# Performance work log

Hardware: AMD Instinct MI355X
Metric: run time of the kernel (lower is better)

Reference implementation:

```python
import jax, jax.numpy as jnp
import numpy as np

DIM = 512
HEADS = 8
DIM_HEAD = 64
INNER = HEADS * DIM_HEAD  # 512
NUM_PATCHES = 64
NUM_FRAMES = 32
EPS = 1e-5


def setup_inputs() -> dict:
    key = jax.random.key(0)
    k1, k2, k3, k4 = jax.random.split(key, 4)
    B, T = 4, NUM_PATCHES * NUM_FRAMES  # 4, 2048
    x = jax.random.normal(k1, (B, T, DIM), dtype=jnp.float32)
    w_qkv = jax.random.normal(k2, (DIM, 3 * INNER), dtype=jnp.float32) * (DIM ** -0.5)
    w_out = jax.random.normal(k3, (INNER, DIM), dtype=jnp.float32) * (INNER ** -0.5)
    b_out = jax.random.normal(k4, (DIM,), dtype=jnp.float32) * 0.01
    ln_g = jnp.ones((DIM,), dtype=jnp.float32)
    ln_b = jnp.zeros((DIM,), dtype=jnp.float32)
    return {"x": x, "ln_g": ln_g, "ln_b": ln_b, "w_qkv": w_qkv, "w_out": w_out, "b_out": b_out}


def _frame_causal_mask(T):
    # token i belongs to frame i // NUM_PATCHES; query frame attends to frames <= its own
    frame = jnp.arange(T) // NUM_PATCHES
    return frame[:, None] >= frame[None, :]  # [T, T] bool


def reference(x, ln_g, ln_b, w_qkv, w_out, b_out):
    B, T, C = x.shape
    scale = DIM_HEAD ** -0.5
    # LayerNorm
    mu = jnp.mean(x, axis=-1, keepdims=True)
    var = jnp.mean(jnp.square(x - mu), axis=-1, keepdims=True)
    xn = (x - mu) * jax.lax.rsqrt(var + EPS) * ln_g + ln_b
    # QKV projection (no bias)
    qkv = xn @ w_qkv  # [B, T, 3*INNER]
    q, k, v = jnp.split(qkv, 3, axis=-1)
    reshape = lambda t: t.reshape(B, T, HEADS, DIM_HEAD).transpose(0, 2, 1, 3)  # b h n d
    q, k, v = reshape(q), reshape(k), reshape(v)
    dots = jnp.einsum('bhqd,bhkd->bhqk', q, k) * scale
    mask = _frame_causal_mask(T)
    dots = jnp.where(mask[None, None], dots, -jnp.inf)
    attn = jax.nn.softmax(dots, axis=-1)
    out = jnp.einsum('bhqk,bhkd->bhqd', attn, v)
    out = out.transpose(0, 2, 1, 3).reshape(B, T, INNER)
    return out @ w_out + b_out
```

## Files before the change

kernel.cpp:

```cpp
#include <hip/hip_runtime.h>

typedef unsigned short u16;
typedef float f32x4 __attribute__((ext_vector_type(4)));
typedef short bf16x8 __attribute__((ext_vector_type(8)));

#define MFMA16(a, b, c) __builtin_amdgcn_mfma_f32_16x16x32_bf16((a), (b), (c), 0, 0, 0)
#define SWZ8(row, off) ((off) ^ (((row) & 7) << 3))

#define CFENCE() asm volatile("" ::: "memory")
#define BARRIER() do { CFENCE(); __builtin_amdgcn_s_barrier(); CFENCE(); } while (0)
#define VMW(n) asm volatile("s_waitcnt vmcnt(" #n ")" ::: "memory")

static __device__ __forceinline__ u16 f2bf(float f) {
  union { float f; unsigned u; } c; c.f = f;
  unsigned r = c.u + 0x7fffu + ((c.u >> 16) & 1u);
  return (u16)(r >> 16);
}

static __device__ __forceinline__ float exp2_hw(float x) {
  float r;
  asm("v_exp_f32 %0, %1" : "=v"(r) : "v"(x));
  return r;
}

static __device__ __forceinline__ unsigned cvtpk(float lo, float hi) {
  unsigned r;
  asm("v_cvt_pk_bf16_f32 %0, %1, %2" : "=v"(r) : "v"(lo), "v"(hi));
  return r;
}

static __device__ __forceinline__ void llds16(u16* l, const u16* g) {
  __builtin_amdgcn_global_load_lds((const __attribute__((address_space(1))) void*)g,
                                   (__attribute__((address_space(3))) void*)l, 16, 0, 0);
}

__global__ __launch_bounds__(256) void prep_weights(
    const float* __restrict__ w_qkv, const float* __restrict__ w_out,
    u16* __restrict__ wqkvT, u16* __restrict__ woutT) {
  __shared__ u16 tile[64][66];
  int bid = blockIdx.x;
  const float* src;
  u16* dst;
  int C, tr, tc;
  if (bid < 192) {
    src = w_qkv; dst = wqkvT; C = 1536;
    tr = (bid & 7) * 64;
    tc = (bid >> 3) * 64;
  } else {
    int b2 = bid - 192;
    src = w_out; dst = woutT; C = 512;
    tr = (b2 & 7) * 64;
    tc = (b2 >> 3) * 64;
  }
  int tid = threadIdx.x;
  int i = tid >> 4;
  int j4 = (tid & 15) * 4;
#pragma unroll
  for (int p = 0; p < 4; ++p) {
    int row = i + p * 16;
    float4 v = *(const float4*)&src[(size_t)(tr + row) * C + tc + j4];
    tile[row][j4 + 0] = f2bf(v.x);
    tile[row][j4 + 1] = f2bf(v.y);
    tile[row][j4 + 2] = f2bf(v.z);
    tile[row][j4 + 3] = f2bf(v.w);
  }
  __syncthreads();
  int j = tid >> 3;
  int i8 = (tid & 7) * 8;
#pragma unroll
  for (int p = 0; p < 2; ++p) {
    int orow = j + p * 32;
    union { u16 h[8]; uint4 q; } o;
#pragma unroll
    for (int s = 0; s < 8; ++s) o.h[s] = tile[i8 + s][orow];
    *(uint4*)&dst[(size_t)(tc + orow) * 512 + tr + i8] = o.q;
  }
}

__global__ __launch_bounds__(256) void ln_kernel(
    const float* __restrict__ x, const float* __restrict__ g,
    const float* __restrict__ be, u16* __restrict__ xn) {
  int row = blockIdx.x * 4 + (threadIdx.x >> 6);
  int lane = threadIdx.x & 63;
  const float4* xr = (const float4*)(x + (size_t)row * 512) + lane * 2;
  float4 v0 = xr[0], v1 = xr[1];
  float s = v0.x + v0.y + v0.z + v0.w + v1.x + v1.y + v1.z + v1.w;
  float ss = v0.x * v0.x + v0.y * v0.y + v0.z * v0.z + v0.w * v0.w +
             v1.x * v1.x + v1.y * v1.y + v1.z * v1.z + v1.w * v1.w;
#pragma unroll
  for (int msk = 32; msk >= 1; msk >>= 1) {
    s += __shfl_xor(s, msk, 64);
    ss += __shfl_xor(ss, msk, 64);
  }
  float mu = s * (1.f / 512.f);
  float var = ss * (1.f / 512.f) - mu * mu;
  float rs = rsqrtf(var + 1e-5f);
  const float4* gp = (const float4*)g + lane * 2;
  const float4* bp = (const float4*)be + lane * 2;
  float4 g0 = gp[0], g1 = gp[1], b0 = bp[0], b1 = bp[1];
  union { u16 h[8]; uint4 q; } o;
  o.h[0] = f2bf((v0.x - mu) * rs * g0.x + b0.x);
  o.h[1] = f2bf((v0.y - mu) * rs * g0.y + b0.y);
  o.h[2] = f2bf((v0.z - mu) * rs * g0.z + b0.z);
  o.h[3] = f2bf((v0.w - mu) * rs * g0.w + b0.w);
  o.h[4] = f2bf((v1.x - mu) * rs * g1.x + b1.x);
  o.h[5] = f2bf((v1.y - mu) * rs * g1.y + b1.y);
  o.h[6] = f2bf((v1.z - mu) * rs * g1.z + b1.z);
  o.h[7] = f2bf((v1.w - mu) * rs * g1.w + b1.w);
  *(uint4*)&xn[(size_t)row * 512 + lane * 8] = o.q;
}

__global__ __launch_bounds__(256) void gemm_qkv(
    const u16* __restrict__ A, const u16* __restrict__ BT,
    u16* __restrict__ qb, u16* __restrict__ kb, u16* __restrict__ vtb) {
  __shared__ u16 lsA[128 * 64], lsB[128 * 64];
  int bid = blockIdx.x;
  int xcd = bid & 7, sq = bid >> 3;
  int m0 = (xcd * 8 + (sq & 7)) * 128;
  int n0 = (sq >> 3) * 128;
  int tid = threadIdx.x;
  int lane = tid & 63, wave = tid >> 6;
  int wm = (wave >> 1) * 64, wn = (wave & 1) * 64;
  int lr = lane & 15, lq = lane >> 4;
  f32x4 acc[4][4] = {};
  for (int kt = 0; kt < 8; ++kt) {
#pragma unroll
    for (int c = 0; c < 4; ++c) {
      int ci = c * 256 + tid;
      int row = ci >> 3, colb = ci & 7;
      int goff = kt * 64 + ((colb * 8) ^ ((row & 7) * 8));
      llds16(&lsA[ci * 8], &A[(size_t)(m0 + row) * 512 + goff]);
      llds16(&lsB[ci * 8], &BT[(size_t)(n0 + row) * 512 + goff]);
    }
    __syncthreads();
#pragma unroll
    for (int ks = 0; ks < 2; ++ks) {
      bf16x8 af[4], bfr[4];
#pragma unroll
      for (int i = 0; i < 4; ++i) {
        int ra = wm + i * 16 + lr;
        af[i] = *(const bf16x8*)&lsA[ra * 64 + SWZ8(ra, ks * 32 + lq * 8)];
        int rb = wn + i * 16 + lr;
        bfr[i] = *(const bf16x8*)&lsB[rb * 64 + SWZ8(rb, ks * 32 + lq * 8)];
      }
#pragma unroll
      for (int i = 0; i < 4; ++i)
#pragma unroll
        for (int j = 0; j < 4; ++j)
          acc[i][j] = MFMA16(af[i], bfr[j], acc[i][j]);
    }
    __syncthreads();
  }
#pragma unroll
  for (int j = 0; j < 4; ++j) {
    int gn = n0 + wn + j * 16 + lr;
    int sec = gn >> 9;
    int h = (gn >> 6) & 7;
    int d = gn & 63;
#pragma unroll
    for (int i = 0; i < 4; ++i) {
      int gm = m0 + wm + i * 16 + lq * 4;
      int b = gm >> 11, t0 = gm & 2047;
      int bh = b * 8 + h;
      if (sec == 0) {
#pragma unroll
        for (int r = 0; r < 4; ++r)
          qb[((size_t)bh * 2048 + t0 + r) * 64 + d] = f2bf(acc[i][j][r] * 0.180336880f);
      } else if (sec == 1) {
#pragma unroll
        for (int r = 0; r < 4; ++r)
          kb[((size_t)bh * 2048 + t0 + r) * 64 + d] = f2bf(acc[i][j][r]);
      } else {
        ushort4 pk;
        pk.x = f2bf(acc[i][j][0]);
        pk.y = f2bf(acc[i][j][1]);
        pk.z = f2bf(acc[i][j][2]);
        pk.w = f2bf(acc[i][j][3]);
        *(ushort4*)&vtb[((size_t)bh * 64 + d) * 2048 + t0] = pk;
      }
    }
  }
}

__global__ __launch_bounds__(256) void attn_kernel(
    const u16* __restrict__ qb, const u16* __restrict__ kb,
    const u16* __restrict__ vtb, u16* __restrict__ ao) {
  int blk = blockIdx.x;
  int xcd = blk & 7;
  int seq = blk >> 3;
  int bh = xcd * 4 + (seq & 3);
  int qf = 31 - (seq >> 2);
  int tid = threadIdx.x, lane = tid & 63, wave = tid >> 6;
  int lr = lane & 15, lq = lane >> 4;
  __shared__ u16 lsK[2][64 * 64], lsV[2][64 * 64];
  __shared__ u16 lsP[4][16 * 64];
  const u16* kfb = kb + (size_t)bh * 2048 * 64;
  const u16* vfb = vtb + (size_t)bh * 64 * 2048;

  int ci0 = tid, ci1 = 256 + tid;
  int r0 = ci0 >> 3, cb0 = ci0 & 7, sw0 = (cb0 * 8) ^ ((r0 & 7) * 8);
  int r1 = ci1 >> 3, cb1 = ci1 & 7, sw1 = (cb1 * 8) ^ ((r1 & 7) * 8);

#define STAGE(buf, kf_)                                                        \
  do {                                                                         \
    const u16* kp = kfb + (size_t)(kf_) * 64 * 64;                             \
    llds16(&lsK[buf][ci0 * 8], &kp[(size_t)r0 * 64 + sw0]);                    \
    llds16(&lsK[buf][ci1 * 8], &kp[(size_t)r1 * 64 + sw1]);                    \
    llds16(&lsV[buf][ci0 * 8], &vfb[(size_t)r0 * 2048 + (kf_) * 64 + sw0]);    \
    llds16(&lsV[buf][ci1 * 8], &vfb[(size_t)r1 * 2048 + (kf_) * 64 + sw1]);    \
  } while (0)

  STAGE(0, 0);

  const u16* qbase = qb + ((size_t)bh * 2048 + qf * 64) * 64;
  int qrow = wave * 16 + lr;
  bf16x8 qa0 = *(const bf16x8*)&qbase[qrow * 64 + lq * 8];
  bf16x8 qa1 = *(const bf16x8*)&qbase[qrow * 64 + 32 + lq * 8];

  f32x4 o[4] = {};
  float m = -1e30f, l = 0.f;
  u16* pw = lsP[wave];

  for (int kf = 0; kf <= qf; ++kf) {
    int cur = kf & 1;
    if (kf < qf) {
      STAGE(cur ^ 1, kf + 1);
      VMW(4);
    } else {
      VMW(0);
    }
    BARRIER();
    f32x4 s[4];
    __builtin_amdgcn_s_setprio(1);
#pragma unroll
    for (int c = 0; c < 4; ++c) {
      int rk = c * 16 + lr;
      bf16x8 k0 = *(const bf16x8*)&lsK[cur][rk * 64 + SWZ8(rk, lq * 8)];
      bf16x8 k1 = *(const bf16x8*)&lsK[cur][rk * 64 + SWZ8(rk, 32 + lq * 8)];
      f32x4 z = {};
      z = MFMA16(k0, qa0, z);
      z = MFMA16(k1, qa1, z);
      s[c] = z;
    }
    __builtin_amdgcn_s_setprio(0);
    float m0 = fmaxf(fmaxf(s[0][0], s[0][1]), fmaxf(s[0][2], s[0][3]));
    float m1 = fmaxf(fmaxf(s[1][0], s[1][1]), fmaxf(s[1][2], s[1][3]));
    float m2 = fmaxf(fmaxf(s[2][0], s[2][1]), fmaxf(s[2][2], s[2][3]));
    float m3 = fmaxf(fmaxf(s[3][0], s[3][1]), fmaxf(s[3][2], s[3][3]));
    float mx = fmaxf(fmaxf(m0, m1), fmaxf(m2, m3));
    mx = fmaxf(mx, __shfl_xor(mx, 16, 64));
    mx = fmaxf(mx, __shfl_xor(mx, 32, 64));
    float mn = fmaxf(m, mx);
    float al = exp2_hw(m - mn);
    m = mn;
    float sum = 0.f;
#pragma unroll
    for (int c = 0; c < 4; ++c) {
#pragma unroll
      for (int r = 0; r < 4; ++r) {
        s[c][r] = exp2_hw(s[c][r] - mn);
        sum += s[c][r];
      }
    }
    sum += __shfl_xor(sum, 16, 64);
    sum += __shfl_xor(sum, 32, 64);
    l = l * al + sum;
    float al0 = __shfl(al, lq * 4 + 0, 64);
    float al1 = __shfl(al, lq * 4 + 1, 64);
    float al2 = __shfl(al, lq * 4 + 2, 64);
    float al3 = __shfl(al, lq * 4 + 3, 64);
#pragma unroll
    for (int oc = 0; oc < 4; ++oc) {
      o[oc][0] *= al0;
      o[oc][1] *= al1;
      o[oc][2] *= al2;
      o[oc][3] *= al3;
    }
#pragma unroll
    for (int c = 0; c < 4; ++c) {
      union { unsigned u[2]; uint2 q2; } pk;
      pk.u[0] = cvtpk(s[c][0], s[c][1]);
      pk.u[1] = cvtpk(s[c][2], s[c][3]);
      *(uint2*)&pw[lr * 64 + ((c * 16 + lq * 4) ^ ((lr & 7) * 8))] = pk.q2;
    }
    bf16x8 pa0 = *(const bf16x8*)&pw[lr * 64 + SWZ8(lr, lq * 8)];
    bf16x8 pa1 = *(const bf16x8*)&pw[lr * 64 + SWZ8(lr, 32 + lq * 8)];
    __builtin_amdgcn_s_setprio(1);
#pragma unroll
    for (int oc = 0; oc < 4; ++oc) {
      int rv = oc * 16 + lr;
      bf16x8 v0 = *(const bf16x8*)&lsV[cur][rv * 64 + SWZ8(rv, lq * 8)];
      bf16x8 v1 = *(const bf16x8*)&lsV[cur][rv * 64 + SWZ8(rv, 32 + lq * 8)];
      o[oc] = MFMA16(pa0, v0, o[oc]);
      o[oc] = MFMA16(pa1, v1, o[oc]);
    }
    __builtin_amdgcn_s_setprio(0);
    BARRIER();
  }
#undef STAGE
  float inv = 1.0f / l;
  float i0 = __shfl(inv, lq * 4 + 0, 64);
  float i1 = __shfl(inv, lq * 4 + 1, 64);
  float i2 = __shfl(inv, lq * 4 + 2, 64);
  float i3 = __shfl(inv, lq * 4 + 3, 64);
  int b = bh >> 3, h = bh & 7;
#pragma unroll
  for (int oc = 0; oc < 4; ++oc) {
    int q = qf * 64 + wave * 16 + lq * 4;
    int col = h * 64 + oc * 16 + lr;
    ao[((size_t)b * 2048 + q + 0) * 512 + col] = f2bf(o[oc][0] * i0);
    ao[((size_t)b * 2048 + q + 1) * 512 + col] = f2bf(o[oc][1] * i1);
    ao[((size_t)b * 2048 + q + 2) * 512 + col] = f2bf(o[oc][2] * i2);
    ao[((size_t)b * 2048 + q + 3) * 512 + col] = f2bf(o[oc][3] * i3);
  }
}

__global__ __launch_bounds__(256) void gemm_out(
    const u16* __restrict__ A, const u16* __restrict__ BT,
    const float* __restrict__ bias, float* __restrict__ out) {
  __shared__ u16 lsA[128 * 64], lsB[128 * 64];
  int bid = blockIdx.x;
  int xcd = bid & 7, sq = bid >> 3;
  int m0 = (xcd * 8 + (sq & 7)) * 128;
  int n0 = (sq >> 3) * 128;
  int tid = threadIdx.x;
  int lane = tid & 63, wave = tid >> 6;
  int wm = (wave >> 1) * 64, wn = (wave & 1) * 64;
  int lr = lane & 15, lq = lane >> 4;
  f32x4 acc[4][4] = {};
  for (int kt = 0; kt < 8; ++kt) {
#pragma unroll
    for (int c = 0; c < 4; ++c) {
      int ci = c * 256 + tid;
      int row = ci >> 3, colb = ci & 7;
      int goff = kt * 64 + ((colb * 8) ^ ((row & 7) * 8));
      llds16(&lsA[ci * 8], &A[(size_t)(m0 + row) * 512 + goff]);
      llds16(&lsB[ci * 8], &BT[(size_t)(n0 + row) * 512 + goff]);
    }
    __syncthreads();
#pragma unroll
    for (int ks = 0; ks < 2; ++ks) {
      bf16x8 af[4], bfr[4];
#pragma unroll
      for (int i = 0; i < 4; ++i) {
        int ra = wm + i * 16 + lr;
        af[i] = *(const bf16x8*)&lsA[ra * 64 + SWZ8(ra, ks * 32 + lq * 8)];
        int rb = wn + i * 16 + lr;
        bfr[i] = *(const bf16x8*)&lsB[rb * 64 + SWZ8(rb, ks * 32 + lq * 8)];
      }
#pragma unroll
      for (int i = 0; i < 4; ++i)
#pragma unroll
        for (int j = 0; j < 4; ++j)
          acc[i][j] = MFMA16(af[i], bfr[j], acc[i][j]);
    }
    __syncthreads();
  }
#pragma unroll
  for (int j = 0; j < 4; ++j) {
    int gn = n0 + wn + j * 16 + lr;
    float bj = bias[gn];
#pragma unroll
    for (int i = 0; i < 4; ++i) {
      int gm = m0 + wm + i * 16 + lq * 4;
#pragma unroll
      for (int r = 0; r < 4; ++r)
        out[(size_t)(gm + r) * 512 + gn] = acc[i][j][r] + bj;
    }
  }
}

extern "C" void kernel_launch(void* const* d_in, const int* in_sizes, int n_in,
                              void* d_out, int out_size, void* d_ws, size_t ws_size,
                              hipStream_t stream) {
  const float* x = (const float*)d_in[0];
  const float* ln_g = (const float*)d_in[1];
  const float* ln_b = (const float*)d_in[2];
  const float* w_qkv = (const float*)d_in[3];
  const float* w_out = (const float*)d_in[4];
  const float* b_out = (const float*)d_in[5];
  float* out = (float*)d_out;
  char* ws = (char*)d_ws;

  u16* xn    = (u16*)(ws + 0);
  u16* wqkvT = (u16*)(ws + 8388608);
  u16* woutT = (u16*)(ws + 9961472);
  u16* qb    = (u16*)(ws + 10485760);
  u16* kb    = (u16*)(ws + 18874368);
  u16* vtb   = (u16*)(ws + 27262976);
  u16* ao    = (u16*)(ws + 35651584);

  prep_weights<<<256, 256, 0, stream>>>(w_qkv, w_out, wqkvT, woutT);
  ln_kernel<<<2048, 256, 0, stream>>>(x, ln_g, ln_b, xn);
  gemm_qkv<<<768, 256, 0, stream>>>(xn, wqkvT, qb, kb, vtb);
  attn_kernel<<<1024, 256, 0, stream>>>(qb, kb, vtb, ao);
  gemm_out<<<256, 256, 0, stream>>>(ao, woutT, b_out, out);
}
```

Baseline: 163.9 us.

## Merge LN and weight prep, stage QKV epilogue via LDS, lazily rescale softmax

Three separate changes. First, the LayerNorm and weight-transpose kernels become one launch, which saves a kernel launch and its tail. Second, the QKV GEMM epilogue now writes the tile to LDS and then stores Q, K and transposed V with 16-byte coalesced writes, replacing scattered 2-byte stores. Third, the attention online softmax skips the rescale of the running max and output whenever the new block max is within 8 (log2 units) of the running max for every lane, which cuts exp and multiply work at the cost of a larger dynamic range in the unnormalised accumulators.

Result: faster. 159.5 us (-2.7%).

```diff
diff --git a/kernel.cpp b/kernel.cpp
--- a/kernel.cpp
+++ b/kernel.cpp
@@ -34,25 +34,59 @@
                                    (__attribute__((address_space(3))) void*)l, 16, 0, 0);
 }
 
-__global__ __launch_bounds__(256) void prep_weights(
+__global__ __launch_bounds__(256) void prep_ln(
+    const float* __restrict__ x, const float* __restrict__ g,
+    const float* __restrict__ be, u16* __restrict__ xn,
     const float* __restrict__ w_qkv, const float* __restrict__ w_out,
     u16* __restrict__ wqkvT, u16* __restrict__ woutT) {
   __shared__ u16 tile[64][66];
   int bid = blockIdx.x;
+  int tid = threadIdx.x;
+  if (bid < 2048) {
+    int row = bid * 4 + (tid >> 6);
+    int lane = tid & 63;
+    const float4* xr = (const float4*)(x + (size_t)row * 512) + lane * 2;
+    float4 v0 = xr[0], v1 = xr[1];
+    float s = v0.x + v0.y + v0.z + v0.w + v1.x + v1.y + v1.z + v1.w;
+    float ss = v0.x * v0.x + v0.y * v0.y + v0.z * v0.z + v0.w * v0.w +
+               v1.x * v1.x + v1.y * v1.y + v1.z * v1.z + v1.w * v1.w;
+#pragma unroll
+    for (int msk = 32; msk >= 1; msk >>= 1) {
+      s += __shfl_xor(s, msk, 64);
+      ss += __shfl_xor(ss, msk, 64);
+    }
+    float mu = s * (1.f / 512.f);
+    float var = ss * (1.f / 512.f) - mu * mu;
+    float rs = rsqrtf(var + 1e-5f);
+    const float4* gp = (const float4*)g + lane * 2;
+    const float4* bp = (const float4*)be + lane * 2;
+    float4 g0 = gp[0], g1 = gp[1], b0 = bp[0], b1 = bp[1];
+    union { u16 h[8]; uint4 q; } o;
+    o.h[0] = f2bf((v0.x - mu) * rs * g0.x + b0.x);
+    o.h[1] = f2bf((v0.y - mu) * rs * g0.y + b0.y);
+    o.h[2] = f2bf((v0.z - mu) * rs * g0.z + b0.z);
+    o.h[3] = f2bf((v0.w - mu) * rs * g0.w + b0.w);
+    o.h[4] = f2bf((v1.x - mu) * rs * g1.x + b1.x);
+    o.h[5] = f2bf((v1.y - mu) * rs * g1.y + b1.y);
+    o.h[6] = f2bf((v1.z - mu) * rs * g1.z + b1.z);
+    o.h[7] = f2bf((v1.w - mu) * rs * g1.w + b1.w);
+    *(uint4*)&xn[(size_t)row * 512 + lane * 8] = o.q;
+    return;
+  }
+  int pb = bid - 2048;
   const float* src;
   u16* dst;
   int C, tr, tc;
-  if (bid < 192) {
+  if (pb < 192) {
     src = w_qkv; dst = wqkvT; C = 1536;
-    tr = (bid & 7) * 64;
-    tc = (bid >> 3) * 64;
+    tr = (pb & 7) * 64;
+    tc = (pb >> 3) * 64;
   } else {
-    int b2 = bid - 192;
+    int b2 = pb - 192;
     src = w_out; dst = woutT; C = 512;
     tr = (b2 & 7) * 64;
     tc = (b2 >> 3) * 64;
   }
-  int tid = threadIdx.x;
   int i = tid >> 4;
   int j4 = (tid & 15) * 4;
 #pragma unroll
@@ -77,47 +111,17 @@
   }
 }
 
-__global__ __launch_bounds__(256) void ln_kernel(
-    const float* __restrict__ x, const float* __restrict__ g,
-    const float* __restrict__ be, u16* __restrict__ xn) {
-  int row = blockIdx.x * 4 + (threadIdx.x >> 6);
-  int lane = threadIdx.x & 63;
-  const float4* xr = (const float4*)(x + (size_t)row * 512) + lane * 2;
-  float4 v0 = xr[0], v1 = xr[1];
-  float s = v0.x + v0.y + v0.z + v0.w + v1.x + v1.y + v1.z + v1.w;
-  float ss = v0.x * v0.x + v0.y * v0.y + v0.z * v0.z + v0.w * v0.w +
-             v1.x * v1.x + v1.y * v1.y + v1.z * v1.z + v1.w * v1.w;
-#pragma unroll
-  for (int msk = 32; msk >= 1; msk >>= 1) {
-    s += __shfl_xor(s, msk, 64);
-    ss += __shfl_xor(ss, msk, 64);
-  }
-  float mu = s * (1.f / 512.f);
-  float var = ss * (1.f / 512.f) - mu * mu;
-  float rs = rsqrtf(var + 1e-5f);
-  const float4* gp = (const float4*)g + lane * 2;
-  const float4* bp = (const float4*)be + lane * 2;
-  float4 g0 = gp[0], g1 = gp[1], b0 = bp[0], b1 = bp[1];
-  union { u16 h[8]; uint4 q; } o;
-  o.h[0] = f2bf((v0.x - mu) * rs * g0.x + b0.x);
-  o.h[1] = f2bf((v0.y - mu) * rs * g0.y + b0.y);
-  o.h[2] = f2bf((v0.z - mu) * rs * g0.z + b0.z);
-  o.h[3] = f2bf((v0.w - mu) * rs * g0.w + b0.w);
-  o.h[4] = f2bf((v1.x - mu) * rs * g1.x + b1.x);
-  o.h[5] = f2bf((v1.y - mu) * rs * g1.y + b1.y);
-  o.h[6] = f2bf((v1.z - mu) * rs * g1.z + b1.z);
-  o.h[7] = f2bf((v1.w - mu) * rs * g1.w + b1.w);
-  *(uint4*)&xn[(size_t)row * 512 + lane * 8] = o.q;
-}
-
 __global__ __launch_bounds__(256) void gemm_qkv(
     const u16* __restrict__ A, const u16* __restrict__ BT,
     u16* __restrict__ qb, u16* __restrict__ kb, u16* __restrict__ vtb) {
-  __shared__ u16 lsA[128 * 64], lsB[128 * 64];
+  __shared__ u16 ls[16384];
+  u16* lsA = ls;
+  u16* lsB = ls + 8192;
   int bid = blockIdx.x;
   int xcd = bid & 7, sq = bid >> 3;
   int m0 = (xcd * 8 + (sq & 7)) * 128;
   int n0 = (sq >> 3) * 128;
+  int sec = n0 >> 9;
   int tid = threadIdx.x;
   int lane = tid & 63, wave = tid >> 6;
   int wm = (wave >> 1) * 64, wn = (wave & 1) * 64;
@@ -151,33 +155,52 @@
     }
     __syncthreads();
   }
-#pragma unroll
-  for (int j = 0; j < 4; ++j) {
-    int gn = n0 + wn + j * 16 + lr;
-    int sec = gn >> 9;
-    int h = (gn >> 6) & 7;
-    int d = gn & 63;
-#pragma unroll
-    for (int i = 0; i < 4; ++i) {
-      int gm = m0 + wm + i * 16 + lq * 4;
-      int b = gm >> 11, t0 = gm & 2047;
-      int bh = b * 8 + h;
-      if (sec == 0) {
-#pragma unroll
-        for (int r = 0; r < 4; ++r)
-          qb[((size_t)bh * 2048 + t0 + r) * 64 + d] = f2bf(acc[i][j][r] * 0.180336880f);
-      } else if (sec == 1) {
-#pragma unroll
-        for (int r = 0; r < 4; ++r)
-          kb[((size_t)bh * 2048 + t0 + r) * 64 + d] = f2bf(acc[i][j][r]);
-      } else {
-        ushort4 pk;
-        pk.x = f2bf(acc[i][j][0]);
-        pk.y = f2bf(acc[i][j][1]);
-        pk.z = f2bf(acc[i][j][2]);
-        pk.w = f2bf(acc[i][j][3]);
-        *(ushort4*)&vtb[((size_t)bh * 64 + d) * 2048 + t0] = pk;
-      }
+  int b = m0 >> 11, t0 = m0 & 2047;
+  float sc = (sec == 0) ? 0.180336880f : 1.0f;
+  if (sec < 2) {
+#pragma unroll
+    for (int i = 0; i < 4; ++i)
+#pragma unroll
+      for (int j = 0; j < 4; ++j) {
+        int col = wn + j * 16 + lr;
+#pragma unroll
+        for (int r = 0; r < 4; ++r) {
+          int row = wm + i * 16 + lq * 4 + r;
+          ls[row * 128 + (col ^ ((row & 7) << 3))] = f2bf(acc[i][j][r] * sc);
+        }
+      }
+    __syncthreads();
+    u16* dst = (sec == 0) ? qb : kb;
+#pragma unroll
+    for (int s = 0; s < 8; ++s) {
+      int li = s * 256 + tid;
+      int row = li >> 4, c8 = (li & 15) * 8;
+      uint4 v = *(uint4*)&ls[row * 128 + (c8 ^ ((row & 7) << 3))];
+      int gn = n0 + c8;
+      int h = (gn >> 6) & 7, d = gn & 63;
+      *(uint4*)&dst[((size_t)(b * 8 + h) * 2048 + t0 + row) * 64 + d] = v;
+    }
+  } else {
+#pragma unroll
+    for (int i = 0; i < 4; ++i)
+#pragma unroll
+      for (int j = 0; j < 4; ++j) {
+        int col = wn + j * 16 + lr;
+#pragma unroll
+        for (int r = 0; r < 4; ++r) {
+          int row = wm + i * 16 + lq * 4 + r;
+          ls[col * 128 + (row ^ ((col & 7) << 3))] = f2bf(acc[i][j][r]);
+        }
+      }
+    __syncthreads();
+#pragma unroll
+    for (int s = 0; s < 8; ++s) {
+      int li = s * 256 + tid;
+      int dcol = li >> 4, t8 = (li & 15) * 8;
+      uint4 v = *(uint4*)&ls[dcol * 128 + (t8 ^ ((dcol & 7) << 3))];
+      int gn = n0 + dcol;
+      int h = (gn >> 6) & 7, d = gn & 63;
+      *(uint4*)&vtb[((size_t)(b * 8 + h) * 64 + d) * 2048 + t0 + t8] = v;
     }
   }
 }
@@ -250,32 +273,35 @@
     float mx = fmaxf(fmaxf(m0, m1), fmaxf(m2, m3));
     mx = fmaxf(mx, __shfl_xor(mx, 16, 64));
     mx = fmaxf(mx, __shfl_xor(mx, 32, 64));
-    float mn = fmaxf(m, mx);
-    float al = exp2_hw(m - mn);
-    m = mn;
+    if (!__all(mx <= m + 8.f)) {
+      float mn = fmaxf(m, mx);
+      float al = exp2_hw(m - mn);
+      m = mn;
+      l *= al;
+      float al0 = __shfl(al, lq * 4 + 0, 64);
+      float al1 = __shfl(al, lq * 4 + 1, 64);
+      float al2 = __shfl(al, lq * 4 + 2, 64);
+      float al3 = __shfl(al, lq * 4 + 3, 64);
+#pragma unroll
+      for (int oc = 0; oc < 4; ++oc) {
+        o[oc][0] *= al0;
+        o[oc][1] *= al1;
+        o[oc][2] *= al2;
+        o[oc][3] *= al3;
+      }
+    }
     float sum = 0.f;
 #pragma unroll
     for (int c = 0; c < 4; ++c) {
 #pragma unroll
       for (int r = 0; r < 4; ++r) {
-        s[c][r] = exp2_hw(s[c][r] - mn);
+        s[c][r] = exp2_hw(s[c][r] - m);
         sum += s[c][r];
       }
     }
     sum += __shfl_xor(sum, 16, 64);
     sum += __shfl_xor(sum, 32, 64);
-    l = l * al + sum;
-    float al0 = __shfl(al, lq * 4 + 0, 64);
-    float al1 = __shfl(al, lq * 4 + 1, 64);
-    float al2 = __shfl(al, lq * 4 + 2, 64);
-    float al3 = __shfl(al, lq * 4 + 3, 64);
-#pragma unroll
-    for (int oc = 0; oc < 4; ++oc) {
-      o[oc][0] *= al0;
-      o[oc][1] *= al1;
-      o[oc][2] *= al2;
-      o[oc][3] *= al3;
-    }
+    l += sum;
 #pragma unroll
     for (int c = 0; c < 4; ++c) {
       union { unsigned u[2]; uint2 q2; } pk;
@@ -390,8 +416,7 @@
   u16* vtb   = (u16*)(ws + 27262976);
   u16* ao    = (u16*)(ws + 35651584);
 
-  prep_weights<<<256, 256, 0, stream>>>(w_qkv, w_out, wqkvT, woutT);
-  ln_kernel<<<2048, 256, 0, stream>>>(x, ln_g, ln_b, xn);
+  prep_ln<<<2304, 256, 0, stream>>>(x, ln_g, ln_b, xn, w_qkv, w_out, wqkvT, woutT);
   gemm_qkv<<<768, 256, 0, stream>>>(xn, wqkvT, qb, kb, vtb);
   attn_kernel<<<1024, 256, 0, stream>>>(qb, kb, vtb, ao);
   gemm_out<<<256, 256, 0, stream>>>(ao, woutT, b_out, out);
```
